# Performance work log

Hardware: AMD Instinct MI355X
Metric: run time of the kernel (lower is better)

The kernel has to match this reference:

```python
import jax, jax.numpy as jnp
import numpy as np

D_MODEL = 1024
NHEAD = 16
D_HEAD = D_MODEL // NHEAD


def setup_inputs() -> dict:
    key = jax.random.key(0)
    ks = jax.random.split(key, 5)
    s_in = 1.0 / np.sqrt(D_MODEL)
    x = jax.random.normal(ks[0], (2, 2048, D_MODEL), dtype=jnp.float32)
    Wqkv = jax.random.uniform(ks[1], (D_MODEL, 3 * D_MODEL), jnp.float32, -s_in, s_in)
    bqkv = jax.random.uniform(ks[2], (3 * D_MODEL,), jnp.float32, -s_in, s_in)
    Wproj = jax.random.uniform(ks[3], (D_MODEL, D_MODEL), jnp.float32, -s_in, s_in)
    bproj = jax.random.uniform(ks[4], (D_MODEL,), jnp.float32, -s_in, s_in)
    return {"x": x, "Wqkv": Wqkv, "bqkv": bqkv, "Wproj": Wproj, "bproj": bproj}


def reference(x, Wqkv, bqkv, Wproj, bproj):
    B, N, D = x.shape
    qkv = x @ Wqkv + bqkv                       # [B, N, 3D]
    q, k, v = jnp.split(qkv, 3, axis=-1)
    # [B, N, D] -> [B, H, N, d]
    def to_heads(t):
        return t.reshape(B, N, NHEAD, D_HEAD).transpose(0, 2, 1, 3)
    q, k, v = to_heads(q), to_heads(k), to_heads(v)
    scale = 1.0 / np.sqrt(D_HEAD).astype(np.float32)
    attn = jnp.einsum('bhqd,bhkd->bhqk', q, k) * scale
    attn = jax.nn.softmax(attn, axis=-1)
    y = jnp.einsum('bhqk,bhkd->bhqd', attn, v)  # [B, H, N, d]
    y = y.transpose(0, 2, 1, 3).reshape(B, N, D)
    return y @ Wproj + bproj
```

## Files before the change

### kernel.cpp

```cpp
#include <hip/hip_runtime.h>
#include <hip/hip_bf16.h>
#include <stdint.h>

typedef __hip_bfloat16 bf16;
typedef __attribute__((ext_vector_type(8))) short short8;
typedef __attribute__((ext_vector_type(4))) float f32x4;

#define QSCALE 0.18033688011f

__device__ __forceinline__ float fast_exp2(float x) {
#if __has_builtin(__builtin_amdgcn_exp2f)
  return __builtin_amdgcn_exp2f(x);
#else
  return exp2f(x);
#endif
}

__device__ __forceinline__ uint32_t pack2_bf16(float a, float b) {
#if __has_builtin(__builtin_amdgcn_cvt_pk_bf16_f32)
  typedef __attribute__((ext_vector_type(2))) __bf16 bf16x2;
  bf16x2 v = __builtin_amdgcn_cvt_pk_bf16_f32(a, b);
  return __builtin_bit_cast(uint32_t, v);
#else
  uint32_t ua = __builtin_bit_cast(uint32_t, a);
  uint32_t ub = __builtin_bit_cast(uint32_t, b);
  ua += 0x7FFF + ((ua >> 16) & 1);
  ub += 0x7FFF + ((ub >> 16) & 1);
  return (ua >> 16) | (ub & 0xFFFF0000u);
#endif
}

__device__ __forceinline__ void gload_lds16(const bf16* g, bf16* l) {
#if __has_builtin(__builtin_amdgcn_global_load_lds)
  __builtin_amdgcn_global_load_lds(
      (const __attribute__((address_space(1))) void*)(uintptr_t)g,
      (__attribute__((address_space(3))) void*)(uint32_t)(uintptr_t)l,
      16, 0, 0);
#else
  int lane = threadIdx.x & 63;
  *(short8*)(l + lane * 8) = *(const short8*)(g + lane * 8);
#endif
}

#define VM4_BARRIER() \
  asm volatile("s_waitcnt vmcnt(4)\n\ts_barrier" ::: "memory")
#define VM3_BARRIER() \
  asm volatile("s_waitcnt vmcnt(3)\n\ts_barrier" ::: "memory")
#define LDSR_BARRIER() \
  asm volatile("s_waitcnt lgkmcnt(0)\n\ts_barrier" ::: "memory")
#define DMA_BARRIER() \
  asm volatile("s_waitcnt vmcnt(0) lgkmcnt(0)\n\ts_barrier" ::: "memory")

__device__ __forceinline__ void transpose_tile(const float* __restrict__ in,
                                               bf16* __restrict__ out,
                                               int R, int C, int bx, int by,
                                               bf16 (*t)[72]) {
  const int r0 = by * 64, c0 = bx * 64;
  const int rr = threadIdx.x >> 3, cc = (threadIdx.x & 7) * 8;
#pragma unroll
  for (int rep = 0; rep < 2; ++rep) {
    int y = rr + rep * 32;
    const float* p = in + (size_t)(r0 + y) * C + c0 + cc;
    f32x4 v0 = *(const f32x4*)p;
    f32x4 v1 = *(const f32x4*)(p + 4);
#pragma unroll
    for (int j = 0; j < 4; ++j) {
      t[cc + j][y] = __float2bfloat16(v0[j]);
      t[cc + 4 + j][y] = __float2bfloat16(v1[j]);
    }
  }
  __syncthreads();
#pragma unroll
  for (int rep = 0; rep < 2; ++rep) {
    int y = rr + rep * 32;
    short8 v = *(const short8*)&t[y][cc];
    *(short8*)(out + (size_t)(c0 + y) * R + r0 + cc) = v;
  }
}

__global__ __launch_bounds__(256)
void prep_k(const float* __restrict__ x, bf16* __restrict__ xb,
            const float* __restrict__ Wqkv, bf16* __restrict__ WtQkv,
            const float* __restrict__ Wproj, bf16* __restrict__ WtP) {
  __shared__ __align__(16) bf16 t[64][72];
  const int bid = blockIdx.x;
  if (bid < 2048) {
    int i = (bid * 256 + threadIdx.x) * 8;
    f32x4 v0 = *(const f32x4*)(x + i);
    f32x4 v1 = *(const f32x4*)(x + i + 4);
    short8 r;
    bf16* rb = (bf16*)&r;
#pragma unroll
    for (int j = 0; j < 4; ++j) {
      rb[j] = __float2bfloat16(v0[j]);
      rb[4 + j] = __float2bfloat16(v1[j]);
    }
    *(short8*)(xb + i) = r;
  } else if (bid < 2048 + 768) {
    int b = bid - 2048;
    transpose_tile(Wqkv, WtQkv, 1024, 3072, b % 48, b / 48, t);
  } else {
    int b = bid - 2816;
    transpose_tile(Wproj, WtP, 1024, 1024, b % 16, b / 16, t);
  }
}

template <int MODE, int TM>
__global__ __launch_bounds__(256, (TM == 128) ? 3 : 2)
void gemm_bt(const bf16* __restrict__ A, const bf16* __restrict__ Bt,
             const float* __restrict__ bias, float* __restrict__ outp,
             bf16* __restrict__ Qd, bf16* __restrict__ Kd, bf16* __restrict__ Vt,
             int M, int Nn, int K) {
  constexpr int MI = TM / 32;
  constexpr int BUFE = TM * 32 + 4096;
  __shared__ __align__(16) bf16 smem[3 * BUFE];

  const int tid = threadIdx.x;
  const int wave = tid >> 6, lane = tid & 63;
  const int quad = lane >> 4, l16 = lane & 15;
  const int mw = (wave >> 1) * (TM / 2), nw = (wave & 1) * 64;

  const int nwg = gridDim.x * gridDim.y;
  const int ord = blockIdx.y * gridDim.x + blockIdx.x;
  const int wg = (ord & 7) * (nwg >> 3) + (ord >> 3);
  const int m_blk = (wg / gridDim.x) * TM, n_blk = (wg % gridDim.x) * 128;

  f32x4 acc[MI][4];
#pragma unroll
  for (int i = 0; i < MI; ++i)
#pragma unroll
    for (int j = 0; j < 4; ++j) acc[i][j] = (f32x4){0.f, 0.f, 0.f, 0.f};

  const int rowA = lane >> 2, colA = (lane & 3) * 8;
  const int chunkB = wave * 2;
  const bf16* gB = Bt + (size_t)(n_blk + chunkB * 16 + rowA) * K + colA;
  const int chunkA = (TM == 128) ? wave * 2 : wave;
  const bf16* gA = A + (size_t)(m_blk + chunkA * 16 + rowA) * K + colA;

  const int oA0 = chunkA * 512;
  const int oA1 = (chunkA + 1) * 512;
  const int oB0 = TM * 32 + chunkB * 512;
  const int oB1 = TM * 32 + (chunkB + 1) * 512;

  const int nI = K >> 5;
  auto issue = [&](int t, int buf) {
    bf16* b = smem + buf * BUFE;
    const int kk = t << 5;
    gload_lds16(gA + kk, b + oA0);
    if (TM == 128) gload_lds16(gA + 16 * K + kk, b + oA1);
    gload_lds16(gB + kk, b + oB0);
    gload_lds16(gB + 16 * K + kk, b + oB1);
  };

  issue(0, 0);
  issue(1, 1);

  for (int it = 0; it < nI; ++it) {
    if constexpr (TM == 128) VM4_BARRIER(); else VM3_BARRIER();

    issue((it + 2 < nI) ? it + 2 : nI - 1, (it + 2) % 3);

    bf16* bufc = smem + (it % 3) * BUFE;
    short8 af[MI], bfv[4];
#pragma unroll
    for (int i = 0; i < MI; ++i)
      af[i] = *(const short8*)&bufc[(mw + i * 16 + l16) * 32 + quad * 8];
#pragma unroll
    for (int j = 0; j < 4; ++j)
      bfv[j] = *(const short8*)&bufc[TM * 32 + (nw + j * 16 + l16) * 32 + quad * 8];
#pragma unroll
    for (int i = 0; i < MI; ++i)
#pragma unroll
      for (int j = 0; j < 4; ++j)
        acc[i][j] = __builtin_amdgcn_mfma_f32_16x16x32_bf16(af[i], bfv[j],
                                                            acc[i][j], 0, 0, 0);
  }

  DMA_BARRIER();

  if (MODE == 0) {
    float bval[4];
#pragma unroll
    for (int j = 0; j < 4; ++j) bval[j] = bias[n_blk + nw + j * 16 + l16];

    const int part = n_blk >> 10;
    const int b = m_blk >> 11;
    const int tloc = m_blk & 2047;
    const int h0 = (n_blk & 1023) >> 6;

#pragma unroll
    for (int p = 0; p < 2; ++p) {
      __syncthreads();
      if ((nw >> 6) == p) {
        if (part == 2) {
#pragma unroll
          for (int i = 0; i < MI; ++i)
#pragma unroll
            for (int j = 0; j < 4; ++j) {
              const int dh = j * 16 + l16;
              const int t0 = mw + i * 16 + quad * 4;
              uint2 pk;
              pk.x = pack2_bf16(acc[i][j][0] + bval[j], acc[i][j][1] + bval[j]);
              pk.y = pack2_bf16(acc[i][j][2] + bval[j], acc[i][j][3] + bval[j]);
              *(uint2*)&smem[dh * 136 + t0] = pk;
            }
        } else {
          const float sc = (part == 0) ? QSCALE : 1.0f;
#pragma unroll
          for (int i = 0; i < MI; ++i)
#pragma unroll
            for (int j = 0; j < 4; ++j) {
              const int d = j * 16 + l16;
              const int t0 = mw + i * 16 + quad * 4;
#pragma unroll
              for (int r = 0; r < 4; ++r)
                smem[(t0 + r) * 72 + d] =
                    __float2bfloat16((acc[i][j][r] + bval[j]) * sc);
            }
        }
      }
      __syncthreads();
      const size_t bh = (size_t)(b * 16 + h0 + p);
      if (part == 2) {
#pragma unroll
        for (int it = 0; it < 4; ++it) {
          const int dl = (tid >> 4) + it * 16;
          const int t8 = (tid & 15) * 8;
          short8 v = *(const short8*)&smem[dl * 136 + t8];
          const int c = (t8 & 63) >> 3;
          const int kvh = c >> 2, cc = c & 3;
          const int q0 = (cc * 2) & 3, q1 = (cc * 2 + 1) & 3;
          const int e2 = cc >> 1;
          const int x7 = dl & 7;
          const size_t rowb = (bh * 64 + dl) * 2048 + tloc + (t8 & 64);
          uint4 u = __builtin_bit_cast(uint4, v);
          *(uint2*)&Vt[rowb + (((kvh * 4 + q0) ^ x7) << 3) + e2 * 4] =
              (uint2){u.x, u.y};
          *(uint2*)&Vt[rowb + (((kvh * 4 + q1) ^ x7) << 3) + e2 * 4] =
              (uint2){u.z, u.w};
        }
      } else {
        bf16* dst = (part == 0) ? Qd : Kd;
#pragma unroll
        for (int it = 0; it < 4; ++it) {
          const int row = (tid >> 3) + it * 32;
          const int col8 = (tid & 7) * 8;
          const int c8 = (part == 1) ? (col8 ^ ((row & 7) << 3)) : col8;
          short8 v = *(const short8*)&smem[row * 72 + col8];
          *(short8*)&dst[(bh * 2048 + tloc + row) * 64 + c8] = v;
        }
      }
    }
  } else {
#pragma unroll
    for (int j = 0; j < 4; ++j) {
      const int ncol = n_blk + nw + j * 16 + l16;
      const float bval = bias[ncol];
#pragma unroll
      for (int i = 0; i < MI; ++i) {
        const int mrow0 = m_blk + mw + i * 16 + quad * 4;
#pragma unroll
        for (int r = 0; r < 4; ++r)
          outp[(size_t)(mrow0 + r) * Nn + ncol] = acc[i][j][r] + bval;
      }
    }
  }
}

__global__ __launch_bounds__(256, 4)
void attn_kernel(const bf16* __restrict__ Qg, const bf16* __restrict__ Kg,
                 const bf16* __restrict__ Vt, bf16* __restrict__ yg) {
  __shared__ __align__(16) char pool[32768];
  bf16* KsB = (bf16*)pool;
  bf16* VtsB = (bf16*)(pool + 16384);

  const int tid = threadIdx.x;
  const int wave = tid >> 6, lane = tid & 63;
  const int quad = lane >> 4, l16 = lane & 15;
  const int qh = wave & 1, kvh = wave >> 1;

  const int bx0 = blockIdx.x;
  const int bx = ((bx0 & 7) << 7) | (bx0 >> 3);
  const int qt = bx & 31;
  const int bh = bx >> 5;

  const bf16* Qb = Qg + ((size_t)bh * 2048 + qt * 64) * 64;
  const bf16* Kb = Kg + (size_t)bh * 2048 * 64;
  const bf16* Vtb = Vt + (size_t)bh * 64 * 2048;

  short8 qf[2][2];
#pragma unroll
  for (int qblk = 0; qblk < 2; ++qblk)
#pragma unroll
    for (int ks = 0; ks < 2; ++ks)
      qf[qblk][ks] = *(const short8*)(
          Qb + (size_t)(qh * 32 + qblk * 16 + l16) * 64 + ks * 32 + quad * 8);

  const int sj = wave * 2;
  const bf16* kg = Kb + sj * 512 + lane * 8;
  const bf16* vg = Vtb + (size_t)(sj * 8 + (lane >> 3)) * 2048 +
                   (lane & 7) * 8;

  int kfo[2][2];
#pragma unroll
  for (int kvblk = 0; kvblk < 2; ++kvblk)
#pragma unroll
    for (int ks = 0; ks < 2; ++ks)
      kfo[kvblk][ks] = (kvh * 32 + kvblk * 16 + l16) * 64 +
                       (((ks * 4 + quad) ^ (l16 & 7)) << 3);
  int vro[4];
#pragma unroll
  for (int dblk = 0; dblk < 4; ++dblk) {
    const int d = dblk * 16 + l16;
    vro[dblk] = d * 64 + (((kvh * 4 + quad) ^ (d & 7)) << 3);
  }

#pragma unroll
  for (int j = 0; j < 2; ++j) {
    gload_lds16(kg + j * 512, KsB + sj * 512 + j * 512);
    gload_lds16(vg + (size_t)j * 16384, VtsB + sj * 512 + j * 512);
  }

  f32x4 yacc[2][4];
#pragma unroll
  for (int qblk = 0; qblk < 2; ++qblk)
#pragma unroll
    for (int dblk = 0; dblk < 4; ++dblk)
      yacc[qblk][dblk] = (f32x4){0.f, 0.f, 0.f, 0.f};
  f32x4 sum_acc[2];
  sum_acc[0] = (f32x4){0.f, 0.f, 0.f, 0.f};
  sum_acc[1] = (f32x4){0.f, 0.f, 0.f, 0.f};

  uint4 ones_u;
  ones_u.x = ones_u.y = ones_u.z = ones_u.w = 0x3F803F80u;
  const short8 ones8 = __builtin_bit_cast(short8, ones_u);

  for (int kt = 0; kt < 2048; kt += 64) {
    const int cur = (kt >> 6) & 1;

    {
      const int kn = (kt + 64 < 2048) ? (kt + 64) : (2048 - 64);
      bf16* Kdst = KsB + (cur ^ 1) * 4096;
      bf16* Vdst = VtsB + (cur ^ 1) * 4096;
#pragma unroll
      for (int j = 0; j < 2; ++j) {
        gload_lds16(kg + kn * 64 + j * 512, Kdst + sj * 512 + j * 512);
        gload_lds16(vg + kn + (size_t)j * 16384, Vdst + sj * 512 + j * 512);
      }
    }

    VM4_BARRIER();

    const bf16* KsC = KsB + cur * 4096;
    const bf16* VtsC = VtsB + cur * 4096;

    short8 kf[2][2];
#pragma unroll
    for (int kvblk = 0; kvblk < 2; ++kvblk)
#pragma unroll
      for (int ks = 0; ks < 2; ++ks)
        kf[kvblk][ks] = *(const short8*)(KsC + kfo[kvblk][ks]);

    short8 pa8[2];
#pragma unroll
    for (int qblk = 0; qblk < 2; ++qblk) {
      f32x4 s0 = (f32x4){0.f, 0.f, 0.f, 0.f};
      f32x4 s1 = (f32x4){0.f, 0.f, 0.f, 0.f};
      s0 = __builtin_amdgcn_mfma_f32_16x16x32_bf16(kf[0][0], qf[qblk][0], s0, 0, 0, 0);
      s0 = __builtin_amdgcn_mfma_f32_16x16x32_bf16(kf[0][1], qf[qblk][1], s0, 0, 0, 0);
      s1 = __builtin_amdgcn_mfma_f32_16x16x32_bf16(kf[1][0], qf[qblk][0], s1, 0, 0, 0);
      s1 = __builtin_amdgcn_mfma_f32_16x16x32_bf16(kf[1][1], qf[qblk][1], s1, 0, 0, 0);
      float p0 = fast_exp2(s0[0]), p1 = fast_exp2(s0[1]);
      float p2 = fast_exp2(s0[2]), p3 = fast_exp2(s0[3]);
      float p4 = fast_exp2(s1[0]), p5 = fast_exp2(s1[1]);
      float p6 = fast_exp2(s1[2]), p7 = fast_exp2(s1[3]);
      uint4 u;
      u.x = pack2_bf16(p0, p1);
      u.y = pack2_bf16(p2, p3);
      u.z = pack2_bf16(p4, p5);
      u.w = pack2_bf16(p6, p7);
      pa8[qblk] = __builtin_bit_cast(short8, u);
      sum_acc[qblk] = __builtin_amdgcn_mfma_f32_16x16x32_bf16(
          pa8[qblk], ones8, sum_acc[qblk], 0, 0, 0);
    }

#pragma unroll
    for (int dblk = 0; dblk < 4; ++dblk) {
      short8 vb8 = *(const short8*)(VtsC + vro[dblk]);
      yacc[0][dblk] = __builtin_amdgcn_mfma_f32_16x16x32_bf16(
          pa8[0], vb8, yacc[0][dblk], 0, 0, 0);
      yacc[1][dblk] = __builtin_amdgcn_mfma_f32_16x16x32_bf16(
          pa8[1], vb8, yacc[1][dblk], 0, 0, 0);
    }

    LDSR_BARRIER();
  }

  DMA_BARRIER();
  float* red = (float*)pool;
  float* sred = (float*)(pool + 16384);
  if (kvh == 1) {
#pragma unroll
    for (int qblk = 0; qblk < 2; ++qblk) {
#pragma unroll
      for (int dblk = 0; dblk < 4; ++dblk) {
        const int f = (qh * 2 + qblk) * 4 + dblk;
        *(f32x4*)&red[(f * 64 + quad * 16 + l16) * 4] = yacc[qblk][dblk];
      }
      if (l16 == 0)
        *(f32x4*)&sred[(qh * 2 + qblk) * 16 + quad * 4] = sum_acc[qblk];
    }
  }
  __syncthreads();
  if (kvh == 0) {
    const int b = bh >> 4, h = bh & 15;
    const size_t rowbase = (size_t)b * 2048 + qt * 64;
#pragma unroll
    for (int qblk = 0; qblk < 2; ++qblk) {
      f32x4 sp = *(const f32x4*)&sred[(qh * 2 + qblk) * 16 + quad * 4];
#pragma unroll
      for (int dblk = 0; dblk < 4; ++dblk) {
        const int f = (qh * 2 + qblk) * 4 + dblk;
        f32x4 o = *(const f32x4*)&red[(f * 64 + quad * 16 + l16) * 4];
#pragma unroll
        for (int r = 0; r < 4; ++r) yacc[qblk][dblk][r] += o[r];
      }
#pragma unroll
      for (int r = 0; r < 4; ++r) {
        const float inv = 1.f / (sum_acc[qblk][r] + sp[r]);
        const int rr = qh * 32 + qblk * 16 + quad * 4 + r;
#pragma unroll
        for (int dblk = 0; dblk < 4; ++dblk)
          yg[(rowbase + rr) * 1024 + h * 64 + dblk * 16 + l16] =
              __float2bfloat16(yacc[qblk][dblk][r] * inv);
      }
    }
  }
}

extern "C" void kernel_launch(void* const* d_in, const int* in_sizes, int n_in,
                              void* d_out, int out_size, void* d_ws, size_t ws_size,
                              hipStream_t stream) {
  const float* x = (const float*)d_in[0];
  const float* Wqkv = (const float*)d_in[1];
  const float* bqkv = (const float*)d_in[2];
  const float* Wproj = (const float*)d_in[3];
  const float* bproj = (const float*)d_in[4];
  float* out = (float*)d_out;

  if (ws_size < (size_t)40 * 1024 * 1024) return;

  char* ws = (char*)d_ws;
  bf16* xb    = (bf16*)(ws + 0);
  bf16* yd    = (bf16*)(ws + 0);
  bf16* WtQkv = (bf16*)(ws + 8388608);
  bf16* WtP   = (bf16*)(ws + 14680064);
  bf16* Qd    = (bf16*)(ws + 16777216);
  bf16* Kd    = (bf16*)(ws + 25165824);
  bf16* Vten  = (bf16*)(ws + 33554432);

  prep_k<<<3072, 256, 0, stream>>>(x, xb, Wqkv, WtQkv, Wproj, WtP);
  gemm_bt<0, 128><<<dim3(24, 32), 256, 0, stream>>>(
      xb, WtQkv, bqkv, nullptr, Qd, Kd, Vten, 4096, 3072, 1024);
  attn_kernel<<<dim3(1024), 256, 0, stream>>>(Qd, Kd, Vten, yd);
  gemm_bt<1, 64><<<dim3(8, 64), 256, 0, stream>>>(
      yd, WtP, bproj, out, nullptr, nullptr, nullptr, 4096, 1024, 1024);
}
```

Baseline: 180.5 us.

## Halve attention query tile to 32 rows and add MFMA wave priority hints

```diff
diff --git a/kernel.cpp b/kernel.cpp
--- a/kernel.cpp
+++ b/kernel.cpp
@@ -42,6 +42,9 @@
 #endif
 }
 
+#define SETPRIO1() __builtin_amdgcn_s_setprio(1)
+#define SETPRIO0() __builtin_amdgcn_s_setprio(0)
+
 #define VM4_BARRIER() \
   asm volatile("s_waitcnt vmcnt(4)\n\ts_barrier" ::: "memory")
 #define VM3_BARRIER() \
@@ -168,12 +171,14 @@
 #pragma unroll
     for (int j = 0; j < 4; ++j)
       bfv[j] = *(const short8*)&bufc[TM * 32 + (nw + j * 16 + l16) * 32 + quad * 8];
+    SETPRIO1();
 #pragma unroll
     for (int i = 0; i < MI; ++i)
 #pragma unroll
       for (int j = 0; j < 4; ++j)
         acc[i][j] = __builtin_amdgcn_mfma_f32_16x16x32_bf16(af[i], bfv[j],
                                                             acc[i][j], 0, 0, 0);
+    SETPRIO0();
   }
 
   DMA_BARRIER();
@@ -267,7 +272,7 @@
   }
 }
 
-__global__ __launch_bounds__(256, 4)
+__global__ __launch_bounds__(256, 5)
 void attn_kernel(const bf16* __restrict__ Qg, const bf16* __restrict__ Kg,
                  const bf16* __restrict__ Vt, bf16* __restrict__ yg) {
   __shared__ __align__(16) char pool[32768];
@@ -280,21 +285,19 @@
   const int qh = wave & 1, kvh = wave >> 1;
 
   const int bx0 = blockIdx.x;
-  const int bx = ((bx0 & 7) << 7) | (bx0 >> 3);
-  const int qt = bx & 31;
-  const int bh = bx >> 5;
-
-  const bf16* Qb = Qg + ((size_t)bh * 2048 + qt * 64) * 64;
+  const int bx = ((bx0 & 7) << 8) | (bx0 >> 3);
+  const int qt = bx & 63;
+  const int bh = bx >> 6;
+
+  const bf16* Qb = Qg + ((size_t)bh * 2048 + qt * 32) * 64;
   const bf16* Kb = Kg + (size_t)bh * 2048 * 64;
   const bf16* Vtb = Vt + (size_t)bh * 64 * 2048;
 
-  short8 qf[2][2];
-#pragma unroll
-  for (int qblk = 0; qblk < 2; ++qblk)
-#pragma unroll
-    for (int ks = 0; ks < 2; ++ks)
-      qf[qblk][ks] = *(const short8*)(
-          Qb + (size_t)(qh * 32 + qblk * 16 + l16) * 64 + ks * 32 + quad * 8);
+  short8 qf[2];
+#pragma unroll
+  for (int ks = 0; ks < 2; ++ks)
+    qf[ks] = *(const short8*)(
+        Qb + (size_t)(qh * 16 + l16) * 64 + ks * 32 + quad * 8);
 
   const int sj = wave * 2;
   const bf16* kg = Kb + sj * 512 + lane * 8;
@@ -321,15 +324,11 @@
     gload_lds16(vg + (size_t)j * 16384, VtsB + sj * 512 + j * 512);
   }
 
-  f32x4 yacc[2][4];
-#pragma unroll
-  for (int qblk = 0; qblk < 2; ++qblk)
-#pragma unroll
-    for (int dblk = 0; dblk < 4; ++dblk)
-      yacc[qblk][dblk] = (f32x4){0.f, 0.f, 0.f, 0.f};
-  f32x4 sum_acc[2];
-  sum_acc[0] = (f32x4){0.f, 0.f, 0.f, 0.f};
-  sum_acc[1] = (f32x4){0.f, 0.f, 0.f, 0.f};
+  f32x4 yacc[4];
+#pragma unroll
+  for (int dblk = 0; dblk < 4; ++dblk)
+    yacc[dblk] = (f32x4){0.f, 0.f, 0.f, 0.f};
+  f32x4 sum_acc = (f32x4){0.f, 0.f, 0.f, 0.f};
 
   uint4 ones_u;
   ones_u.x = ones_u.y = ones_u.z = ones_u.w = 0x3F803F80u;
@@ -361,37 +360,35 @@
       for (int ks = 0; ks < 2; ++ks)
         kf[kvblk][ks] = *(const short8*)(KsC + kfo[kvblk][ks]);
 
-    short8 pa8[2];
-#pragma unroll
-    for (int qblk = 0; qblk < 2; ++qblk) {
-      f32x4 s0 = (f32x4){0.f, 0.f, 0.f, 0.f};
-      f32x4 s1 = (f32x4){0.f, 0.f, 0.f, 0.f};
-      s0 = __builtin_amdgcn_mfma_f32_16x16x32_bf16(kf[0][0], qf[qblk][0], s0, 0, 0, 0);
-      s0 = __builtin_amdgcn_mfma_f32_16x16x32_bf16(kf[0][1], qf[qblk][1], s0, 0, 0, 0);
-      s1 = __builtin_amdgcn_mfma_f32_16x16x32_bf16(kf[1][0], qf[qblk][0], s1, 0, 0, 0);
-      s1 = __builtin_amdgcn_mfma_f32_16x16x32_bf16(kf[1][1], qf[qblk][1], s1, 0, 0, 0);
-      float p0 = fast_exp2(s0[0]), p1 = fast_exp2(s0[1]);
-      float p2 = fast_exp2(s0[2]), p3 = fast_exp2(s0[3]);
-      float p4 = fast_exp2(s1[0]), p5 = fast_exp2(s1[1]);
-      float p6 = fast_exp2(s1[2]), p7 = fast_exp2(s1[3]);
-      uint4 u;
-      u.x = pack2_bf16(p0, p1);
-      u.y = pack2_bf16(p2, p3);
-      u.z = pack2_bf16(p4, p5);
-      u.w = pack2_bf16(p6, p7);
-      pa8[qblk] = __builtin_bit_cast(short8, u);
-      sum_acc[qblk] = __builtin_amdgcn_mfma_f32_16x16x32_bf16(
-          pa8[qblk], ones8, sum_acc[qblk], 0, 0, 0);
-    }
-
+    SETPRIO1();
+    f32x4 s0 = (f32x4){0.f, 0.f, 0.f, 0.f};
+    f32x4 s1 = (f32x4){0.f, 0.f, 0.f, 0.f};
+    s0 = __builtin_amdgcn_mfma_f32_16x16x32_bf16(kf[0][0], qf[0], s0, 0, 0, 0);
+    s0 = __builtin_amdgcn_mfma_f32_16x16x32_bf16(kf[0][1], qf[1], s0, 0, 0, 0);
+    s1 = __builtin_amdgcn_mfma_f32_16x16x32_bf16(kf[1][0], qf[0], s1, 0, 0, 0);
+    s1 = __builtin_amdgcn_mfma_f32_16x16x32_bf16(kf[1][1], qf[1], s1, 0, 0, 0);
+    SETPRIO0();
+    float p0 = fast_exp2(s0[0]), p1 = fast_exp2(s0[1]);
+    float p2 = fast_exp2(s0[2]), p3 = fast_exp2(s0[3]);
+    float p4 = fast_exp2(s1[0]), p5 = fast_exp2(s1[1]);
+    float p6 = fast_exp2(s1[2]), p7 = fast_exp2(s1[3]);
+    uint4 u;
+    u.x = pack2_bf16(p0, p1);
+    u.y = pack2_bf16(p2, p3);
+    u.z = pack2_bf16(p4, p5);
+    u.w = pack2_bf16(p6, p7);
+    const short8 pa8 = __builtin_bit_cast(short8, u);
+    sum_acc = __builtin_amdgcn_mfma_f32_16x16x32_bf16(pa8, ones8, sum_acc,
+                                                      0, 0, 0);
+
+    SETPRIO1();
 #pragma unroll
     for (int dblk = 0; dblk < 4; ++dblk) {
       short8 vb8 = *(const short8*)(VtsC + vro[dblk]);
-      yacc[0][dblk] = __builtin_amdgcn_mfma_f32_16x16x32_bf16(
-          pa8[0], vb8, yacc[0][dblk], 0, 0, 0);
-      yacc[1][dblk] = __builtin_amdgcn_mfma_f32_16x16x32_bf16(
-          pa8[1], vb8, yacc[1][dblk], 0, 0, 0);
-    }
+      yacc[dblk] = __builtin_amdgcn_mfma_f32_16x16x32_bf16(
+          pa8, vb8, yacc[dblk], 0, 0, 0);
+    }
+    SETPRIO0();
 
     LDSR_BARRIER();
   }
@@ -401,39 +398,32 @@
   float* sred = (float*)(pool + 16384);
   if (kvh == 1) {
 #pragma unroll
-    for (int qblk = 0; qblk < 2; ++qblk) {
-#pragma unroll
-      for (int dblk = 0; dblk < 4; ++dblk) {
-        const int f = (qh * 2 + qblk) * 4 + dblk;
-        *(f32x4*)&red[(f * 64 + quad * 16 + l16) * 4] = yacc[qblk][dblk];
-      }
-      if (l16 == 0)
-        *(f32x4*)&sred[(qh * 2 + qblk) * 16 + quad * 4] = sum_acc[qblk];
-    }
+    for (int dblk = 0; dblk < 4; ++dblk) {
+      const int f = qh * 4 + dblk;
+      *(f32x4*)&red[(f * 64 + lane) * 4] = yacc[dblk];
+    }
+    if (l16 == 0) *(f32x4*)&sred[qh * 16 + quad * 4] = sum_acc;
   }
   __syncthreads();
   if (kvh == 0) {
     const int b = bh >> 4, h = bh & 15;
-    const size_t rowbase = (size_t)b * 2048 + qt * 64;
-#pragma unroll
-    for (int qblk = 0; qblk < 2; ++qblk) {
-      f32x4 sp = *(const f32x4*)&sred[(qh * 2 + qblk) * 16 + quad * 4];
-#pragma unroll
-      for (int dblk = 0; dblk < 4; ++dblk) {
-        const int f = (qh * 2 + qblk) * 4 + dblk;
-        f32x4 o = *(const f32x4*)&red[(f * 64 + quad * 16 + l16) * 4];
-#pragma unroll
-        for (int r = 0; r < 4; ++r) yacc[qblk][dblk][r] += o[r];
-      }
-#pragma unroll
-      for (int r = 0; r < 4; ++r) {
-        const float inv = 1.f / (sum_acc[qblk][r] + sp[r]);
-        const int rr = qh * 32 + qblk * 16 + quad * 4 + r;
-#pragma unroll
-        for (int dblk = 0; dblk < 4; ++dblk)
-          yg[(rowbase + rr) * 1024 + h * 64 + dblk * 16 + l16] =
-              __float2bfloat16(yacc[qblk][dblk][r] * inv);
-      }
+    const size_t rowbase = (size_t)b * 2048 + qt * 32;
+    f32x4 sp = *(const f32x4*)&sred[qh * 16 + quad * 4];
+#pragma unroll
+    for (int dblk = 0; dblk < 4; ++dblk) {
+      const int f = qh * 4 + dblk;
+      f32x4 o = *(const f32x4*)&red[(f * 64 + lane) * 4];
+#pragma unroll
+      for (int r = 0; r < 4; ++r) yacc[dblk][r] += o[r];
+    }
+#pragma unroll
+    for (int r = 0; r < 4; ++r) {
+      const float inv = 1.f / (sum_acc[r] + sp[r]);
+      const int rr = qh * 16 + quad * 4 + r;
+#pragma unroll
+      for (int dblk = 0; dblk < 4; ++dblk)
+        yg[(rowbase + rr) * 1024 + h * 64 + dblk * 16 + l16] =
+            __float2bfloat16(yacc[dblk][r] * inv);
     }
   }
 }
@@ -462,7 +452,7 @@
   prep_k<<<3072, 256, 0, stream>>>(x, xb, Wqkv, WtQkv, Wproj, WtP);
   gemm_bt<0, 128><<<dim3(24, 32), 256, 0, stream>>>(
       xb, WtQkv, bqkv, nullptr, Qd, Kd, Vten, 4096, 3072, 1024);
-  attn_kernel<<<dim3(1024), 256, 0, stream>>>(Qd, Kd, Vten, yd);
+  attn_kernel<<<dim3(2048), 256, 0, stream>>>(Qd, Kd, Vten, yd);
   gemm_bt<1, 64><<<dim3(8, 64), 256, 0, stream>>>(
       yd, WtP, bproj, out, nullptr, nullptr, nullptr, 4096, 1024, 1024);
 }
```

Result: slower. 192.5 us (+6.6%).
